# Kernel optimization log

Hardware: AMD Instinct MI355X
Metric: run time of the kernel (lower is better)

The kernel has to match this reference:

```python
import jax, jax.numpy as jnp
import numpy as np
from jax import lax

V, VE, DE, DX, HID, T, S = 100000, 1000, 256, 64, 512, 64, 2048
H = HID // 2


def setup_inputs() -> dict:
    key = jax.random.key(0)
    ks = jax.random.split(key, 18)
    def n(k, shape, scale=0.1):
        return jax.random.normal(k, shape, jnp.float32) * scale
    return {
        "sentence": jax.random.randint(ks[0], (S,), 0, V),
        "extra": jax.random.randint(ks[1], (S,), 0, VE),
        "b": 0,
        "e": S,
        "emb": n(ks[2], (V, DE)),
        "extra_emb": n(ks[3], (VE, DX)),
        "w_ih_f": n(ks[4], (4 * H, DE + DX)),
        "w_hh_f": n(ks[5], (4 * H, H)),
        "b_ih_f": n(ks[6], (4 * H,)),
        "b_hh_f": n(ks[7], (4 * H,)),
        "w_ih_b": n(ks[8], (4 * H, DE + DX)),
        "w_hh_b": n(ks[9], (4 * H, H)),
        "b_ih_b": n(ks[10], (4 * H,)),
        "b_hh_b": n(ks[11], (4 * H,)),
        "fc_w": n(ks[12], (T, HID)),
        "fc_b": n(ks[13], (T,)),
        "crf_start": n(ks[14], (T,)),
        "crf_end": n(ks[15], (T,)),
        "crf_trans": n(ks[16], (T, T)),
    }


def _lstm_dir(x, w_ih, w_hh, b_ih, b_hh):
    """Single-direction LSTM over x [S, D] with batch 1. PyTorch gate order i,f,g,o."""
    Hh = w_hh.shape[1]
    gx = x @ w_ih.T + (b_ih + b_hh)  # [S, 4H], input projection hoisted out of the scan

    def step(carry, g_in):
        h, c = carry
        g = g_in + h @ w_hh.T  # [4H]
        i, f, gg, o = jnp.split(g, 4)
        i = jax.nn.sigmoid(i)
        f = jax.nn.sigmoid(f)
        gg = jnp.tanh(gg)
        o = jax.nn.sigmoid(o)
        c = f * c + i * gg
        h = o * jnp.tanh(c)
        return (h, c), h

    init = (jnp.zeros((Hh,), x.dtype), jnp.zeros((Hh,), x.dtype))
    _, hs = lax.scan(step, init, gx)
    return hs  # [S, H]


def _lstm_feats(sentence, extra, emb, extra_emb,
                w_ih_f, w_hh_f, b_ih_f, b_hh_f,
                w_ih_b, w_hh_b, b_ih_b, b_hh_b, fc_w, fc_b):
    x = jnp.concatenate([emb[sentence], extra_emb[extra]], axis=1)  # [S, DE+DX]
    hf = _lstm_dir(x, w_ih_f, w_hh_f, b_ih_f, b_hh_f)              # [S, H]
    hb = _lstm_dir(x[::-1], w_ih_b, w_hh_b, b_ih_b, b_hh_b)[::-1]  # [S, H]
    lstm_out = jnp.concatenate([hf, hb], axis=1)                   # [S, 2H]
    return lstm_out @ fc_w.T + fc_b                                # [S, T]


def _viterbi_decode(feats, start, end, trans):
    """torchcrf-style Viterbi on feats [L, T]; returns best tag path [L] (int32)."""
    score0 = start + feats[0]  # [T]

    def step(score, emit_t):
        m = score[:, None] + trans + emit_t[None, :]  # [T_prev, T_next]
        return jnp.max(m, axis=0), jnp.argmax(m, axis=0).astype(jnp.int32)

    final_score, bps = lax.scan(step, score0, feats[1:])  # bps: [L-1, T]
    final_score = final_score + end
    last_tag = jnp.argmax(final_score).astype(jnp.int32)

    def back(tag, bp_t):
        prev = bp_t[tag]
        return prev, prev

    _, prev_tags = lax.scan(back, last_tag, bps[::-1])
    return jnp.concatenate([prev_tags[::-1], last_tag[None]])  # [L]


def reference(sentence, extra, b, e, emb, extra_emb,
              w_ih_f, w_hh_f, b_ih_f, b_hh_f,
              w_ih_b, w_hh_b, b_ih_b, b_hh_b,
              fc_w, fc_b, crf_start, crf_end, crf_trans):
    feats = _lstm_feats(sentence, extra, emb, extra_emb,
                        w_ih_f, w_hh_f, b_ih_f, b_hh_f,
                        w_ih_b, w_hh_b, b_ih_b, b_hh_b, fc_w, fc_b)
    feats = feats[b:e]  # static Python-int phrase bounds
    return _viterbi_decode(feats, crf_start, crf_end, crf_trans)
```

## Files before the change

kernel.cpp:

```cpp
#include <hip/hip_runtime.h>
#include <stdint.h>

#define SEQ   2048
#define DE    256
#define DXX   64
#define DIN   320
#define HH    256
#define G4    1024
#define NT    64

static constexpr size_t OFF_GX = 0;
static constexpr size_t OFF_H  = OFF_GX + (size_t)2 * SEQ * G4;
static constexpr size_t HSTR   = (size_t)SEQ * HH;
static constexpr size_t OFF_SL = OFF_H + 2 * HSTR;
static constexpr size_t OFF_FE = OFF_SL + 1024;
static constexpr size_t OFF_BP = OFF_FE + (size_t)SEQ * NT;
static constexpr size_t WS_NEEDED_BYTES = OFF_BP * 4 + (size_t)SEQ * NT;

__global__ __launch_bounds__(256) void k_init(unsigned long long* __restrict__ slot) {
  const int tid = threadIdx.x;
  slot[tid] = 0ull;
  slot[256 + tid] = 0ull;
}

__global__ __launch_bounds__(512) void k_gx(
    const int* __restrict__ sent, const int* __restrict__ extra,
    const float* __restrict__ emb, const float* __restrict__ xemb,
    const float* __restrict__ wf, const float* __restrict__ wb,
    const float* __restrict__ bif, const float* __restrict__ bhf,
    const float* __restrict__ bib, const float* __restrict__ bhb,
    float* __restrict__ GX) {
  __shared__ __align__(16) float xs[32][36];
  __shared__ __align__(16) float wl[32][260];
  const int tid = threadIdx.x;
  const int s0 = blockIdx.x * 32, r0 = blockIdx.y * 256, dir = blockIdx.z;
  const float* W = dir ? wb : wf;
  const int tids = tid & 7;
  const int tidr = tid >> 3;
  float acc[4][4];
  #pragma unroll
  for (int a = 0; a < 4; ++a)
    #pragma unroll
    for (int b = 0; b < 4; ++b) acc[a][b] = 0.f;

  for (int kc = 0; kc < 10; ++kc) {
    const int k0 = kc * 32;
    __syncthreads();
    for (int e = tid; e < 1024; e += 512) {
      int kk = e & 31, sl = e >> 5;
      int s = s0 + sl;
      int src = dir ? (SEQ - 1 - s) : s;
      int k = k0 + kk;
      float v;
      if (k < DE) v = emb[(size_t)sent[src] * DE + k];
      else        v = xemb[(size_t)extra[src] * DXX + (k - DE)];
      xs[kk][sl] = v;
    }
    for (int e = tid; e < 8192; e += 512) {
      int kk = e & 31, rl = e >> 5;
      wl[kk][rl] = W[(size_t)(r0 + rl) * DIN + k0 + kk];
    }
    __syncthreads();
    #pragma unroll
    for (int kk = 0; kk < 32; ++kk) {
      float4 xv = *(const float4*)&xs[kk][4 * tids];
      float4 wv = *(const float4*)&wl[kk][4 * tidr];
      acc[0][0] += xv.x * wv.x; acc[0][1] += xv.x * wv.y; acc[0][2] += xv.x * wv.z; acc[0][3] += xv.x * wv.w;
      acc[1][0] += xv.y * wv.x; acc[1][1] += xv.y * wv.y; acc[1][2] += xv.y * wv.z; acc[1][3] += xv.y * wv.w;
      acc[2][0] += xv.z * wv.x; acc[2][1] += xv.z * wv.y; acc[2][2] += xv.z * wv.z; acc[2][3] += xv.z * wv.w;
      acc[3][0] += xv.w * wv.x; acc[3][1] += xv.w * wv.y; acc[3][2] += xv.w * wv.z; acc[3][3] += xv.w * wv.w;
    }
  }
  const float* BI = dir ? bib : bif;
  const float* BH = dir ? bhb : bhf;
  float4 b1 = *(const float4*)&BI[r0 + 4 * tidr];
  float4 b2 = *(const float4*)&BH[r0 + 4 * tidr];
  float bx = b1.x + b2.x, by = b1.y + b2.y, bz = b1.z + b2.z, bw = b1.w + b2.w;
  #pragma unroll
  for (int ss = 0; ss < 4; ++ss) {
    int s = s0 + 4 * tids + ss;
    float4 o;
    o.x = acc[ss][0] + bx; o.y = acc[ss][1] + by; o.z = acc[ss][2] + bz; o.w = acc[ss][3] + bw;
    *(float4*)&GX[((size_t)dir * SEQ + s) * G4 + r0 + 4 * tidr] = o;
  }
}

__global__ __launch_bounds__(512, 2) void k_lstm_tag(
    const float* __restrict__ whf, const float* __restrict__ whb,
    const float* __restrict__ GX, float* __restrict__ H,
    unsigned long long* __restrict__ slot) {
  const int dir = blockIdx.x >> 2;
  const int p   = blockIdx.x & 3;
  const int tid = threadIdx.x;
  const int half = tid >> 8;
  const int r    = tid & 255;
  const int gi = r >> 6, l = r & 63;
  const int j   = (p << 6) | l;
  const int row = (gi << 8) | j;
  const float4* w4g =
      (const float4*)((dir ? whb : whf) + (size_t)row * HH) + half * 32;
  float4 w[32];
  #pragma unroll
  for (int i = 0; i < 32; ++i) w[i] = w4g[i];
  const float* gxp = GX + (size_t)dir * SEQ * G4 + row;
  float* Hd = H + (size_t)dir * HSTR;
  unsigned long long* sl = slot + dir * 256;

  __shared__ __align__(16) float hl[HH];
  __shared__ float ps[2][256];
  __shared__ float gl[4][64];
  float c = 0.f;
  int budget = 1 << 18;

  for (int t = 0; t < SEQ; ++t) {
    float gxv = 0.f;
    if (half == 0) gxv = gxp[(size_t)t * G4];
    if (tid < 256) {
      unsigned long long v;
      do {
        v = __hip_atomic_load(&sl[tid], __ATOMIC_RELAXED,
                              __HIP_MEMORY_SCOPE_AGENT);
      } while ((unsigned)(v >> 32) != (unsigned)t && --budget > 0);
      union { unsigned u; float f; } cv; cv.u = (unsigned)v;
      hl[tid] = cv.f;
    }
    __syncthreads();
    const float4* h4 = (const float4*)hl + half * 32;
    float a0 = 0.f, a1 = 0.f, a2 = 0.f, a3 = 0.f;
    #pragma unroll
    for (int i = 0; i < 32; ++i) {
      float4 wv = w[i];
      float4 hv = h4[i];
      a0 += wv.x * hv.x; a1 += wv.y * hv.y; a2 += wv.z * hv.z; a3 += wv.w * hv.w;
    }
    ps[half][r] = (a0 + a1) + (a2 + a3);
    __syncthreads();
    if (tid < 256) {
      float acc = gxv + (ps[0][tid] + ps[1][tid]);
      gl[tid >> 6][tid & 63] = acc;
    }
    __syncthreads();
    if (tid < 64) {
      float iv = gl[0][tid], fv = gl[1][tid], gv = gl[2][tid], ov = gl[3][tid];
      float ig = 1.f / (1.f + expf(-iv));
      float fg = 1.f / (1.f + expf(-fv));
      float gg = tanhf(gv);
      float og = 1.f / (1.f + expf(-ov));
      c = fg * c + ig * gg;
      float h = og * tanhf(c);
      int jj = (p << 6) | tid;
      Hd[(size_t)t * HH + jj] = h;
      union { float f; unsigned u; } hu; hu.f = h;
      unsigned long long pk =
          ((unsigned long long)(unsigned)(t + 1) << 32) | hu.u;
      __hip_atomic_store(&sl[jj], pk, __ATOMIC_RELAXED,
                         __HIP_MEMORY_SCOPE_AGENT);
    }
  }
}

__global__ __launch_bounds__(256) void k_feats(
    const float* __restrict__ HF, const float* __restrict__ HB,
    const float* __restrict__ fcw, const float* __restrict__ fcb,
    float* __restrict__ FE) {
  __shared__ float hlds[16][512];
  __shared__ float wl[64][65];
  const int tid = threadIdx.x;
  const int s0 = blockIdx.x * 16;
  for (int e = tid; e < 16 * 512; e += 256) {
    int sl = e >> 9, k = e & 511;
    float v = (k < HH) ? HF[(size_t)(s0 + sl) * HH + k]
                       : HB[(size_t)(SEQ - 1 - (s0 + sl)) * HH + (k - HH)];
    hlds[sl][k] = v;
  }
  const int j = tid & 63, sg = tid >> 6;
  float acc[4];
  #pragma unroll
  for (int q = 0; q < 4; ++q) acc[q] = fcb[j];
  for (int kc = 0; kc < 8; ++kc) {
    __syncthreads();
    for (int e = tid; e < 4096; e += 256) {
      int kk = e & 63, jj = e >> 6;
      wl[kk][jj] = fcw[(size_t)jj * 512 + kc * 64 + kk];
    }
    __syncthreads();
    #pragma unroll 8
    for (int kk = 0; kk < 64; ++kk) {
      float wv = wl[kk][j];
      int kg = kc * 64 + kk;
      #pragma unroll
      for (int q = 0; q < 4; ++q) acc[q] += hlds[4 * sg + q][kg] * wv;
    }
  }
  #pragma unroll
  for (int q = 0; q < 4; ++q)
    FE[(size_t)(s0 + 4 * sg + q) * NT + j] = acc[q];
}

__global__ __launch_bounds__(256) void k_viterbi(
    const float* __restrict__ feats, const float* __restrict__ start,
    const float* __restrict__ endv, const float* __restrict__ trans,
    unsigned char* __restrict__ bp, int* __restrict__ out) {
  __shared__ float tr[64 * 64];
  __shared__ float sc[64];
  __shared__ float pval[4][64];
  __shared__ int pidx[4][64];
  const int tid = threadIdx.x;
  for (int e = tid; e < 4096; e += 256) tr[e] = trans[e];
  if (tid < 64) sc[tid] = start[tid] + feats[tid];
  __syncthreads();
  const int w = tid >> 6, j = tid & 63;
  for (int t = 1; t < SEQ; ++t) {
    float fj = feats[t * NT + j];
    float best = -3.0e38f; int bi = 0;
    const int ibase = w << 4;
    #pragma unroll
    for (int ii = 0; ii < 16; ++ii) {
      int i = ibase + ii;
      float v = (sc[i] + tr[(i << 6) | j]) + fj;
      if (v > best) { best = v; bi = i; }
    }
    pval[w][j] = best; pidx[w][j] = bi;
    __syncthreads();
    if (w == 0) {
      float b = pval[0][j]; int x = pidx[0][j];
      if (pval[1][j] > b) { b = pval[1][j]; x = pidx[1][j]; }
      if (pval[2][j] > b) { b = pval[2][j]; x = pidx[2][j]; }
      if (pval[3][j] > b) { b = pval[3][j]; x = pidx[3][j]; }
      bp[t * NT + j] = (unsigned char)x;
      sc[j] = b;
    }
    __syncthreads();
  }
  if (tid == 0) {
    float best = -3.0e38f; int bt = 0;
    for (int i = 0; i < 64; ++i) {
      float v = sc[i] + endv[i];
      if (v > best) { best = v; bt = i; }
    }
    out[SEQ - 1] = bt;
    int tag = bt;
    for (int t = SEQ - 1; t >= 1; --t) {
      tag = bp[t * NT + tag];
      out[t - 1] = tag;
    }
  }
}

extern "C" void kernel_launch(void* const* d_in, const int* in_sizes, int n_in,
                              void* d_out, int out_size, void* d_ws, size_t ws_size,
                              hipStream_t stream) {
  if (n_in < 19) return;
  if (in_sizes[0] != SEQ || in_sizes[1] != SEQ) return;
  if (in_sizes[2] != 1 || in_sizes[3] != 1) return;
  if (in_sizes[4] != 100000 * DE) return;
  if (in_sizes[5] != 1000 * DXX) return;
  if (in_sizes[6] != G4 * DIN || in_sizes[7] != G4 * HH) return;
  if (in_sizes[8] != G4 || in_sizes[9] != G4) return;
  if (in_sizes[10] != G4 * DIN || in_sizes[11] != G4 * HH) return;
  if (in_sizes[14] != NT * 512 || in_sizes[15] != NT) return;
  if (in_sizes[16] != NT || in_sizes[17] != NT) return;
  if (in_sizes[18] != NT * NT) return;
  if (out_size < SEQ) return;
  if (ws_size < WS_NEEDED_BYTES) return;

  const int*   sent = (const int*)d_in[0];
  const int*   extra = (const int*)d_in[1];
  const float* emb  = (const float*)d_in[4];
  const float* xemb = (const float*)d_in[5];
  const float* wihf = (const float*)d_in[6];
  const float* whhf = (const float*)d_in[7];
  const float* bihf = (const float*)d_in[8];
  const float* bhhf = (const float*)d_in[9];
  const float* wihb = (const float*)d_in[10];
  const float* whhb = (const float*)d_in[11];
  const float* bihb = (const float*)d_in[12];
  const float* bhhb = (const float*)d_in[13];
  const float* fcw  = (const float*)d_in[14];
  const float* fcb  = (const float*)d_in[15];
  const float* cst  = (const float*)d_in[16];
  const float* cen  = (const float*)d_in[17];
  const float* ctr  = (const float*)d_in[18];

  float* ws = (float*)d_ws;
  float* GX = ws + OFF_GX;
  float* H  = ws + OFF_H;
  unsigned long long* SLOT = (unsigned long long*)(ws + OFF_SL);
  float* FE = ws + OFF_FE;
  unsigned char* BP = (unsigned char*)(ws + OFF_BP);

  k_init<<<1, 256, 0, stream>>>(SLOT);
  k_gx<<<dim3(SEQ / 32, G4 / 256, 2), 512, 0, stream>>>(
      sent, extra, emb, xemb, wihf, wihb, bihf, bhhf, bihb, bhhb, GX);
  k_lstm_tag<<<8, 512, 0, stream>>>(whhf, whhb, GX, H, SLOT);
  k_feats<<<SEQ / 16, 256, 0, stream>>>(H, H + HSTR, fcw, fcb, FE);
  k_viterbi<<<1, 256, 0, stream>>>(FE, cst, cen, ctr, BP, (int*)d_out);
}
```

Measured before the change: 6.057 ms.

## Split LSTM recurrence across 16 blocks per direction with double-buffered h slots

Spreads the recurrent LSTM step over 16 workgroups per direction (32 total) instead of 4, with each thread holding a quarter of a weight row and a four-way shared-memory reduction. The h exchange slots become double-buffered by timestep parity, so a fast producer does not overwrite values a slow consumer is still reading. The aim is less per-step matvec latency per block, in exchange for more blocks polling global memory each step and possibly more cross-block synchronization latency.

```diff
diff --git a/kernel.cpp b/kernel.cpp
--- a/kernel.cpp
+++ b/kernel.cpp
@@ -13,14 +13,14 @@
 static constexpr size_t OFF_H  = OFF_GX + (size_t)2 * SEQ * G4;
 static constexpr size_t HSTR   = (size_t)SEQ * HH;
 static constexpr size_t OFF_SL = OFF_H + 2 * HSTR;
-static constexpr size_t OFF_FE = OFF_SL + 1024;
+static constexpr size_t OFF_FE = OFF_SL + 2048;
 static constexpr size_t OFF_BP = OFF_FE + (size_t)SEQ * NT;
 static constexpr size_t WS_NEEDED_BYTES = OFF_BP * 4 + (size_t)SEQ * NT;
 
 __global__ __launch_bounds__(256) void k_init(unsigned long long* __restrict__ slot) {
   const int tid = threadIdx.x;
-  slot[tid] = 0ull;
-  slot[256 + tid] = 0ull;
+  #pragma unroll
+  for (int b = 0; b < 4; ++b) slot[b * 256 + tid] = 0ull;
 }
 
 __global__ __launch_bounds__(512) void k_gx(
@@ -85,75 +85,83 @@
   }
 }
 
-__global__ __launch_bounds__(512, 2) void k_lstm_tag(
+__global__ __launch_bounds__(256, 1) void k_lstm16(
     const float* __restrict__ whf, const float* __restrict__ whb,
     const float* __restrict__ GX, float* __restrict__ H,
     unsigned long long* __restrict__ slot) {
-  const int dir = blockIdx.x >> 2;
-  const int p   = blockIdx.x & 3;
-  const int tid = threadIdx.x;
-  const int half = tid >> 8;
-  const int r    = tid & 255;
-  const int gi = r >> 6, l = r & 63;
-  const int j   = (p << 6) | l;
-  const int row = (gi << 8) | j;
+  const int dir = blockIdx.x >> 4;
+  const int p   = blockIdx.x & 15;
+  const int tid = threadIdx.x;
+  const int rr  = tid >> 2;
+  const int q   = tid & 3;
+  const int gq  = rr >> 4;
+  const int joq = rr & 15;
+  const int rowQ = (gq << 8) | (p << 4) | joq;
+  const int rowC = ((tid >> 4) << 8) | (p << 4) | (tid & 15);
+
   const float4* w4g =
-      (const float4*)((dir ? whb : whf) + (size_t)row * HH) + half * 32;
-  float4 w[32];
-  #pragma unroll
-  for (int i = 0; i < 32; ++i) w[i] = w4g[i];
-  const float* gxp = GX + (size_t)dir * SEQ * G4 + row;
+      (const float4*)((dir ? whb : whf) + (size_t)rowQ * HH) + q * 16;
+  float4 w[16];
+  #pragma unroll
+  for (int i = 0; i < 16; ++i) w[i] = w4g[i];
+  #pragma unroll
+  for (int i = 0; i < 16; ++i)
+    asm volatile("" : "+v"(w[i].x), "+v"(w[i].y), "+v"(w[i].z), "+v"(w[i].w));
+
+  const float* gxc = GX + (size_t)dir * SEQ * G4 + rowC;
   float* Hd = H + (size_t)dir * HSTR;
-  unsigned long long* sl = slot + dir * 256;
+  unsigned long long* sl = slot + dir * 512;
 
   __shared__ __align__(16) float hl[HH];
-  __shared__ float ps[2][256];
-  __shared__ float gl[4][64];
+  __shared__ float psum[256];
+  __shared__ float gacc[64];
   float c = 0.f;
   int budget = 1 << 18;
 
   for (int t = 0; t < SEQ; ++t) {
     float gxv = 0.f;
-    if (half == 0) gxv = gxp[(size_t)t * G4];
-    if (tid < 256) {
+    if (tid < 64) gxv = gxc[(size_t)t * G4];
+    {
+      unsigned long long* sp = &sl[(t & 1) * 256 + tid];
       unsigned long long v;
       do {
-        v = __hip_atomic_load(&sl[tid], __ATOMIC_RELAXED,
-                              __HIP_MEMORY_SCOPE_AGENT);
+        v = __hip_atomic_load(sp, __ATOMIC_RELAXED, __HIP_MEMORY_SCOPE_AGENT);
       } while ((unsigned)(v >> 32) != (unsigned)t && --budget > 0);
       union { unsigned u; float f; } cv; cv.u = (unsigned)v;
       hl[tid] = cv.f;
     }
     __syncthreads();
-    const float4* h4 = (const float4*)hl + half * 32;
+    const float4* h4 = (const float4*)hl + q * 16;
     float a0 = 0.f, a1 = 0.f, a2 = 0.f, a3 = 0.f;
     #pragma unroll
-    for (int i = 0; i < 32; ++i) {
+    for (int i = 0; i < 16; ++i) {
       float4 wv = w[i];
       float4 hv = h4[i];
       a0 += wv.x * hv.x; a1 += wv.y * hv.y; a2 += wv.z * hv.z; a3 += wv.w * hv.w;
     }
-    ps[half][r] = (a0 + a1) + (a2 + a3);
-    __syncthreads();
-    if (tid < 256) {
-      float acc = gxv + (ps[0][tid] + ps[1][tid]);
-      gl[tid >> 6][tid & 63] = acc;
-    }
+    psum[tid] = (a0 + a1) + (a2 + a3);
     __syncthreads();
     if (tid < 64) {
-      float iv = gl[0][tid], fv = gl[1][tid], gv = gl[2][tid], ov = gl[3][tid];
+      float s = gxv + ((psum[4 * tid] + psum[4 * tid + 1]) +
+                       (psum[4 * tid + 2] + psum[4 * tid + 3]));
+      gacc[tid] = s;
+    }
+    __syncthreads();
+    if (tid < 16) {
+      float iv = gacc[tid], fv = gacc[16 + tid], gv = gacc[32 + tid],
+            ov = gacc[48 + tid];
       float ig = 1.f / (1.f + expf(-iv));
       float fg = 1.f / (1.f + expf(-fv));
       float gg = tanhf(gv);
       float og = 1.f / (1.f + expf(-ov));
       c = fg * c + ig * gg;
       float h = og * tanhf(c);
-      int jj = (p << 6) | tid;
+      int jj = (p << 4) | tid;
       Hd[(size_t)t * HH + jj] = h;
       union { float f; unsigned u; } hu; hu.f = h;
       unsigned long long pk =
           ((unsigned long long)(unsigned)(t + 1) << 32) | hu.u;
-      __hip_atomic_store(&sl[jj], pk, __ATOMIC_RELAXED,
+      __hip_atomic_store(&sl[((t + 1) & 1) * 256 + jj], pk, __ATOMIC_RELAXED,
                          __HIP_MEMORY_SCOPE_AGENT);
     }
   }
@@ -292,7 +300,7 @@
   k_init<<<1, 256, 0, stream>>>(SLOT);
   k_gx<<<dim3(SEQ / 32, G4 / 256, 2), 512, 0, stream>>>(
       sent, extra, emb, xemb, wihf, wihb, bihf, bhhf, bihb, bhhb, GX);
-  k_lstm_tag<<<8, 512, 0, stream>>>(whhf, whhb, GX, H, SLOT);
+  k_lstm16<<<32, 256, 0, stream>>>(whhf, whhb, GX, H, SLOT);
   k_feats<<<SEQ / 16, 256, 0, stream>>>(H, H + HSTR, fcw, fcb, FE);
   k_viterbi<<<1, 256, 0, stream>>>(FE, cst, cen, ctr, BP, (int*)d_out);
 }
```

Result: faster. 5.511 ms (-9.0%).
